# Kernel optimization log

Hardware: AMD Instinct MI355X
Metric: run time of the kernel (lower is better)

The kernel has to match this reference:

```python
import jax, jax.numpy as jnp
import numpy as np

N, E, D_IN, D, H, L, D_EMB, T = 4096, 131072, 72, 256, 8, 2, 128, 5
HD = D // H
LN_EPS = 1e-5


def _linear(x, w, b):
    # torch Linear: w is [out, in]
    return x @ w.T + b


def _layernorm(x, g, b):
    mu = jnp.mean(x, axis=-1, keepdims=True)
    var = jnp.var(x, axis=-1, keepdims=True)
    return (x - mu) * jax.lax.rsqrt(var + LN_EPS) * g + b


def _gps_layer(x, edge_index, p):
    src, dst = edge_index[0], edge_index[1]
    # GINConv: sum-aggregate neighbor messages, then MLP((1+eps)*x + agg)
    agg = jax.ops.segment_sum(x[src], dst, num_segments=N)
    h = (1.0 + p['gin_eps']) * x + agg
    h = _linear(jax.nn.elu(_linear(h, p['mlp_w1'], p['mlp_b1'])), p['mlp_w2'], p['mlp_b2'])
    h = jax.nn.elu(_layernorm(h, p['ln1_g'], p['ln1_b']))
    x = x + h

    # global multi-head self-attention over all N nodes (seq len = N)
    qkv = x @ p['attn_in_w'].T + p['attn_in_b']  # [N, 3D]
    q, k, v = jnp.split(qkv, 3, axis=-1)
    q = q.reshape(N, H, HD)
    k = k.reshape(N, H, HD)
    v = v.reshape(N, H, HD)
    scores = jnp.einsum('nhd,mhd->hnm', q, k) / np.sqrt(HD).astype(np.float32)
    attn = jax.nn.softmax(scores, axis=-1)
    o = jnp.einsum('hnm,mhd->nhd', attn, v).reshape(N, D)
    o = _linear(o, p['attn_out_w'], p['attn_out_b'])
    o = _layernorm(o, p['ln2_g'], p['ln2_b'])
    x = x + o

    # FFN (dim -> 2*dim -> dim, GELU)
    f = _linear(jax.nn.gelu(_linear(x, p['ffn_w1'], p['ffn_b1'])), p['ffn_w2'], p['ffn_b2'])
    f = _layernorm(f, p['ln3_g'], p['ln3_b'])
    return x + f


def setup_inputs() -> dict:
    key = jax.random.key(0)
    ks = iter(jax.random.split(key, 64))

    def w(shape, fan_in):
        return jax.random.normal(next(ks), shape, jnp.float32) * (1.0 / np.sqrt(fan_in))

    inp = {
        'x': jax.random.normal(next(ks), (N, D_IN), jnp.float32),
        'edge_index': jax.random.randint(next(ks), (2, E), 0, N, jnp.int64),
        'in_w': w((D, D_IN), D_IN), 'in_b': jnp.zeros((D,), jnp.float32),
        'head_w1': w((D_EMB, D), D), 'head_b1': jnp.zeros((D_EMB,), jnp.float32),
        'head_w2': w((T, D_EMB), D_EMB), 'head_b2': jnp.zeros((T,), jnp.float32),
    }
    # stacked per-layer params, leading axis L
    inp['mlp_w1'] = w((L, D, D), D); inp['mlp_b1'] = jnp.zeros((L, D), jnp.float32)
    inp['mlp_w2'] = w((L, D, D), D); inp['mlp_b2'] = jnp.zeros((L, D), jnp.float32)
    inp['gin_eps'] = jnp.zeros((L,), jnp.float32)
    inp['ln1_g'] = jnp.ones((L, D), jnp.float32); inp['ln1_b'] = jnp.zeros((L, D), jnp.float32)
    inp['attn_in_w'] = w((L, 3 * D, D), D); inp['attn_in_b'] = jnp.zeros((L, 3 * D), jnp.float32)
    inp['attn_out_w'] = w((L, D, D), D); inp['attn_out_b'] = jnp.zeros((L, D), jnp.float32)
    inp['ln2_g'] = jnp.ones((L, D), jnp.float32); inp['ln2_b'] = jnp.zeros((L, D), jnp.float32)
    inp['ffn_w1'] = w((L, 2 * D, D), D); inp['ffn_b1'] = jnp.zeros((L, 2 * D), jnp.float32)
    inp['ffn_w2'] = w((L, D, 2 * D), 2 * D); inp['ffn_b2'] = jnp.zeros((L, D), jnp.float32)
    inp['ln3_g'] = jnp.ones((L, D), jnp.float32); inp['ln3_b'] = jnp.zeros((L, D), jnp.float32)
    return inp


PER_LAYER = ['mlp_w1', 'mlp_b1', 'mlp_w2', 'mlp_b2', 'gin_eps', 'ln1_g', 'ln1_b',
             'attn_in_w', 'attn_in_b', 'attn_out_w', 'attn_out_b', 'ln2_g', 'ln2_b',
             'ffn_w1', 'ffn_b1', 'ffn_w2', 'ffn_b2', 'ln3_g', 'ln3_b']


def reference(x, edge_index, in_w, in_b, head_w1, head_b1, head_w2, head_b2,
              mlp_w1, mlp_b1, mlp_w2, mlp_b2, gin_eps, ln1_g, ln1_b,
              attn_in_w, attn_in_b, attn_out_w, attn_out_b, ln2_g, ln2_b,
              ffn_w1, ffn_b1, ffn_w2, ffn_b2, ln3_g, ln3_b):
    stacked = dict(mlp_w1=mlp_w1, mlp_b1=mlp_b1, mlp_w2=mlp_w2, mlp_b2=mlp_b2,
                   gin_eps=gin_eps, ln1_g=ln1_g, ln1_b=ln1_b,
                   attn_in_w=attn_in_w, attn_in_b=attn_in_b,
                   attn_out_w=attn_out_w, attn_out_b=attn_out_b,
                   ln2_g=ln2_g, ln2_b=ln2_b, ffn_w1=ffn_w1, ffn_b1=ffn_b1,
                   ffn_w2=ffn_w2, ffn_b2=ffn_b2, ln3_g=ln3_g, ln3_b=ln3_b)
    h = jax.nn.elu(_linear(x, in_w, in_b))  # input_proj (dropout/noise off in eval)
    for l in range(L):
        p = {k: v[l] for k, v in stacked.items()}
        h = _gps_layer(h, edge_index, p)
    out = _linear(jax.nn.elu(_linear(h, head_w1, head_b1)), head_w2, head_b2)
    return out
```

## Files before the change

### kernel.cpp

```cpp
#include <hip/hip_runtime.h>
#include <math.h>

#define NN 4096
#define NE 131072
#define DIM 256
#define NHEAD 8
#define HD 32

typedef __attribute__((ext_vector_type(8))) short short8v;
typedef __attribute__((ext_vector_type(4))) float f32x4;
#define MFMA16(a, b, c) __builtin_amdgcn_mfma_f32_16x16x32_bf16(a, b, c, 0, 0, 0)

__device__ __forceinline__ float elu_f(float v){ return v > 0.f ? v : expm1f(v); }
__device__ __forceinline__ float gelu_f(float v){
  const float c = 0.7978845608028654f;
  float t = tanhf(c * (v + 0.044715f * v * v * v));
  return 0.5f * v * (1.f + t);
}
__device__ __forceinline__ unsigned short f2bf(float f) {
  unsigned int u = __builtin_bit_cast(unsigned int, f);
  u += 0x7FFFu + ((u >> 16) & 1u);
  return (unsigned short)(u >> 16);
}
__device__ __forceinline__ float bf2f(unsigned short u) {
  return __builtin_bit_cast(float, (unsigned int)u << 16);
}
__device__ __forceinline__ unsigned int pk2(float a, float b) {
  return (unsigned int)f2bf(a) | ((unsigned int)f2bf(b) << 16);
}

__global__ void zero_counts(int* __restrict__ counts) {
  int i = blockIdx.x * 256 + threadIdx.x;
  if (i < NN) counts[i] = 0;
}

__global__ void count_edges(const int* __restrict__ ei, int* __restrict__ counts) {
  int e = blockIdx.x * 256 + threadIdx.x;
  if (e < NE) atomicAdd(&counts[ei[NE + e]], 1);
}

__global__ __launch_bounds__(1024) void scan_offsets(const int* __restrict__ counts,
                                                     int* __restrict__ offs,
                                                     int* __restrict__ cursor) {
  __shared__ int tmp[1024];
  int t = threadIdx.x;
  int base = t * 4;
  int c0 = counts[base], c1 = counts[base+1], c2 = counts[base+2], c3 = counts[base+3];
  int tsum = c0 + c1 + c2 + c3;
  tmp[t] = tsum;
  __syncthreads();
  for (int d = 1; d < 1024; d <<= 1) {
    int v = (t >= d) ? tmp[t - d] : 0;
    __syncthreads();
    tmp[t] += v;
    __syncthreads();
  }
  int excl = tmp[t] - tsum;
  offs[base]   = excl;           cursor[base]   = excl;
  offs[base+1] = excl + c0;      cursor[base+1] = excl + c0;
  offs[base+2] = excl + c0 + c1; cursor[base+2] = excl + c0 + c1;
  offs[base+3] = excl + c0 + c1 + c2; cursor[base+3] = excl + c0 + c1 + c2;
  if (t == 1023) offs[NN] = tmp[1023];
}

__global__ void scatter_edges(const int* __restrict__ ei, int* __restrict__ cursor,
                              int* __restrict__ esrc) {
  int e = blockIdx.x * 256 + threadIdx.x;
  if (e < NE) {
    int d = ei[NE + e];
    int pos = atomicAdd(&cursor[d], 1);
    esrc[pos] = ei[e];
  }
}

__global__ __launch_bounds__(256) void gin_agg(const int* __restrict__ offs,
                                               const int* __restrict__ esrc,
                                               const unsigned short* __restrict__ xb,
                                               const float* __restrict__ eps_p, int l,
                                               unsigned short* __restrict__ aggb) {
  int n = blockIdx.x, c = threadIdx.x;
  int e0 = offs[n], e1 = offs[n + 1];
  float acc = 0.f;
  for (int e = e0; e < e1; e++) acc += bf2f(xb[(size_t)esrc[e] * DIM + c]);
  float eps = eps_p[l];
  aggb[(size_t)n * DIM + c] = f2bf((1.f + eps) * bf2f(xb[(size_t)n * DIM + c]) + acc);
}

template<int ACT, int WF32, int WBF16, int QSCALE, int BK>
__global__ __launch_bounds__(256) void gemm_mfma(
    const unsigned short* __restrict__ A, const unsigned short* __restrict__ W,
    const float* __restrict__ bias, float* __restrict__ Cf,
    unsigned short* __restrict__ Cb, int M, int N, int K)
{
  __shared__ __align__(16) unsigned short As[64][BK + 8];
  __shared__ __align__(16) unsigned short Ws[32][BK + 8];
  constexpr int CPR = BK / 8;
  int t = threadIdx.x;
  int w = t >> 6, lane = t & 63, lo = lane & 15, g = lane >> 4;
  int wm = w & 1, wn = w >> 1;
  int bn = blockIdx.x * 32, bm = blockIdx.y * 64;

  f32x4 acc0 = {0.f, 0.f, 0.f, 0.f};
  f32x4 acc1 = {0.f, 0.f, 0.f, 0.f};

  for (int k0 = 0; k0 < K; k0 += BK) {
    #pragma unroll
    for (int c = 0; c < 64 * CPR; c += 256) {
      int cc = c + t;
      int row = cc / CPR, off = (cc % CPR) * 8;
      *(short8v*)&As[row][off] = *(const short8v*)(A + (size_t)(bm + row) * K + k0 + off);
    }
    {
      int cc = t;
      if (cc < 32 * CPR) {
        int row = cc / CPR, off = (cc % CPR) * 8;
        *(short8v*)&Ws[row][off] = *(const short8v*)(W + (size_t)(bn + row) * K + k0 + off);
      }
    }
    __syncthreads();
    #pragma unroll
    for (int ks = 0; ks < BK; ks += 32) {
      short8v a0 = *(const short8v*)&As[wm * 32 + lo][ks + 8 * g];
      short8v a1 = *(const short8v*)&As[wm * 32 + 16 + lo][ks + 8 * g];
      short8v b0 = *(const short8v*)&Ws[wn * 16 + lo][ks + 8 * g];
      acc0 = MFMA16(a0, b0, acc0);
      acc1 = MFMA16(a1, b0, acc1);
    }
    __syncthreads();
  }

  #pragma unroll
  for (int mi = 0; mi < 2; mi++) {
    f32x4 av = (mi == 0) ? acc0 : acc1;
    #pragma unroll
    for (int r = 0; r < 4; r++) {
      int row = bm + wm * 32 + mi * 16 + 4 * g + r;
      int col = bn + wn * 16 + lo;
      float v = av[r] + bias[col];
      if (ACT == 1) v = elu_f(v);
      if (ACT == 2) v = gelu_f(v);
      if (QSCALE) { if (col < 256) v *= 0.17677669529663687f; }
      if (WF32) Cf[(size_t)row * N + col] = v;
      if (WBF16) Cb[(size_t)row * N + col] = f2bf(v);
    }
  }
}

template<int ACT>
__global__ __launch_bounds__(256) void ln_act_add(const float* __restrict__ in,
                                                  const float* __restrict__ g,
                                                  const float* __restrict__ b,
                                                  float* __restrict__ x,
                                                  unsigned short* __restrict__ xb) {
  int rowb = blockIdx.x;
  int c = threadIdx.x;
  float v = in[(size_t)rowb * DIM + c];
  float s = v, s2 = v * v;
  #pragma unroll
  for (int off = 32; off >= 1; off >>= 1) {
    s  += __shfl_xor(s,  off, 64);
    s2 += __shfl_xor(s2, off, 64);
  }
  __shared__ float ws1[4], ws2[4];
  int w = threadIdx.x >> 6, lane = threadIdx.x & 63;
  if (lane == 0) { ws1[w] = s; ws2[w] = s2; }
  __syncthreads();
  s  = ws1[0] + ws1[1] + ws1[2] + ws1[3];
  s2 = ws2[0] + ws2[1] + ws2[2] + ws2[3];
  float mean = s * (1.f / DIM);
  float var = s2 * (1.f / DIM) - mean * mean;
  float r = rsqrtf(var + 1e-5f);
  float o = (v - mean) * r * g[c] + b[c];
  if (ACT == 1) o = elu_f(o);
  float nx = x[(size_t)rowb * DIM + c] + o;
  x[(size_t)rowb * DIM + c] = nx;
  xb[(size_t)rowb * DIM + c] = f2bf(nx);
}

__global__ __launch_bounds__(256) void vt_transpose(const unsigned short* __restrict__ tbb,
                                                    unsigned short* __restrict__ VT) {
  __shared__ unsigned short lds[128][33];
  int h = blockIdx.y;
  int nb = blockIdx.x * 128;
  int tid = threadIdx.x;
  int r8 = tid >> 5, d = tid & 31;
  #pragma unroll
  for (int i = 0; i < 16; i++) {
    int n = i * 8 + r8;
    lds[n][d] = tbb[(size_t)(nb + n) * 768 + 512 + h * 32 + d];
  }
  __syncthreads();
  int dd = tid >> 7, j = tid & 127;
  #pragma unroll
  for (int i = 0; i < 16; i++) {
    int d2 = i * 2 + dd;
    VT[((size_t)h * 32 + d2) * 4096 + nb + j] = lds[j][d2];
  }
}

__global__ __launch_bounds__(256) void attn_mfma_split(
    const unsigned short* __restrict__ qkvb, const unsigned short* __restrict__ VT,
    float* __restrict__ po, float* __restrict__ ml, int kspan) {
  __shared__ __align__(16) unsigned short Ks[2][64][40];
  __shared__ __align__(16) unsigned short Vs[2][32][72];
  int tid = threadIdx.x;
  int w = tid >> 6, lane = tid & 63;
  int lo = lane & 15, g = lane >> 4;
  int h = blockIdx.y;
  int s = blockIdx.z;
  int qb = blockIdx.x * 64 + w * 16;
  int k_lo = s * kspan, k_hi = k_lo + kspan;

  int krow = tid >> 2, kq = (tid & 3) * 8;
  int vrow = tid >> 3, vo = (tid & 7) * 8;
  const unsigned short* Kg = qkvb + 256 + h * 32;
  const unsigned short* Vg = VT + ((size_t)(h * 32 + vrow)) * 4096;

  short8v qf = *(const short8v*)(qkvb + (size_t)(qb + lo) * 768 + h * 32 + 8 * g);

  f32x4 acc0 = {0.f, 0.f, 0.f, 0.f};
  f32x4 acc1 = {0.f, 0.f, 0.f, 0.f};
  float m = -1e30f, l = 0.f;
  const f32x4 zf = {0.f, 0.f, 0.f, 0.f};

  {
    short8v rk0 = *(const short8v*)(Kg + (size_t)(k_lo + krow) * 768 + kq);
    short8v rv0 = *(const short8v*)(Vg + k_lo + vo);
    *(short8v*)&Ks[0][krow][kq] = rk0;
    *(short8v*)&Vs[0][vrow][vo] = rv0;
  }
  __syncthreads();

  int buf = 0;
  for (int kb = k_lo; kb < k_hi; kb += 64) {
    short8v rk, rv;
    bool more = (kb + 64 < k_hi);
    if (more) {
      rk = *(const short8v*)(Kg + (size_t)(kb + 64 + krow) * 768 + kq);
      rv = *(const short8v*)(Vg + kb + 64 + vo);
    }

    short8v kA0 = *(const short8v*)&Ks[buf][lo][8 * g];
    short8v kA1 = *(const short8v*)&Ks[buf][16 + lo][8 * g];
    short8v kA2 = *(const short8v*)&Ks[buf][32 + lo][8 * g];
    short8v kA3 = *(const short8v*)&Ks[buf][48 + lo][8 * g];
    f32x4 s0_ = MFMA16(kA0, qf, zf);
    f32x4 s1_ = MFMA16(kA1, qf, zf);
    f32x4 s2_ = MFMA16(kA2, qf, zf);
    f32x4 s3_ = MFMA16(kA3, qf, zf);

    float ta_ = fmaxf(fmaxf(fmaxf(s0_[0],s0_[1]), fmaxf(s0_[2],s0_[3])),
                      fmaxf(fmaxf(s1_[0],s1_[1]), fmaxf(s1_[2],s1_[3])));
    float tb_ = fmaxf(fmaxf(fmaxf(s2_[0],s2_[1]), fmaxf(s2_[2],s2_[3])),
                      fmaxf(fmaxf(s3_[0],s3_[1]), fmaxf(s3_[2],s3_[3])));
    float t_ = fmaxf(ta_, tb_);
    t_ = fmaxf(t_, __shfl_xor(t_, 16, 64));
    t_ = fmaxf(t_, __shfl_xor(t_, 32, 64));
    if (!__all(t_ <= m)) {
      float nm_ = fmaxf(m, t_);
      float f_ = __expf(m - nm_);
      m = nm_; l *= f_;
      acc0[0]*=f_; acc0[1]*=f_; acc0[2]*=f_; acc0[3]*=f_;
      acc1[0]*=f_; acc1[1]*=f_; acc1[2]*=f_; acc1[3]*=f_;
    }
    float p0_=__expf(s0_[0]-m), p1_=__expf(s0_[1]-m), p2_=__expf(s0_[2]-m), p3_=__expf(s0_[3]-m);
    float p4_=__expf(s1_[0]-m), p5_=__expf(s1_[1]-m), p6_=__expf(s1_[2]-m), p7_=__expf(s1_[3]-m);
    float p8_=__expf(s2_[0]-m), p9_=__expf(s2_[1]-m), pA_=__expf(s2_[2]-m), pB_=__expf(s2_[3]-m);
    float pC_=__expf(s3_[0]-m), pD_=__expf(s3_[1]-m), pE_=__expf(s3_[2]-m), pF_=__expf(s3_[3]-m);
    l += ((((p0_+p1_)+(p2_+p3_)) + ((p4_+p5_)+(p6_+p7_))) +
          (((p8_+p9_)+(pA_+pB_)) + ((pC_+pD_)+(pE_+pF_))));

    uint4 uA_ = { pk2(p0_,p1_), pk2(p2_,p3_), pk2(p4_,p5_), pk2(p6_,p7_) };
    uint4 uB_ = { pk2(p8_,p9_), pk2(pA_,pB_), pk2(pC_,pD_), pk2(pE_,pF_) };
    short8v pbA_ = __builtin_bit_cast(short8v, uA_);
    short8v pbB_ = __builtin_bit_cast(short8v, uB_);

    short4 Wa0 = *(const short4*)&Vs[buf][lo][4 * g];
    short4 Wa1 = *(const short4*)&Vs[buf][lo][16 + 4 * g];
    short4 Wa2 = *(const short4*)&Vs[buf][lo][32 + 4 * g];
    short4 Wa3 = *(const short4*)&Vs[buf][lo][48 + 4 * g];
    short4 Xa0 = *(const short4*)&Vs[buf][16 + lo][4 * g];
    short4 Xa1 = *(const short4*)&Vs[buf][16 + lo][16 + 4 * g];
    short4 Xa2 = *(const short4*)&Vs[buf][16 + lo][32 + 4 * g];
    short4 Xa3 = *(const short4*)&Vs[buf][16 + lo][48 + 4 * g];
    short8v va0_ = {Wa0.x,Wa0.y,Wa0.z,Wa0.w, Wa1.x,Wa1.y,Wa1.z,Wa1.w};
    short8v va1_ = {Wa2.x,Wa2.y,Wa2.z,Wa2.w, Wa3.x,Wa3.y,Wa3.z,Wa3.w};
    short8v vb0_ = {Xa0.x,Xa0.y,Xa0.z,Xa0.w, Xa1.x,Xa1.y,Xa1.z,Xa1.w};
    short8v vb1_ = {Xa2.x,Xa2.y,Xa2.z,Xa2.w, Xa3.x,Xa3.y,Xa3.z,Xa3.w};
    acc0 = MFMA16(va0_, pbA_, acc0);
    acc0 = MFMA16(va1_, pbB_, acc0);
    acc1 = MFMA16(vb0_, pbA_, acc1);
    acc1 = MFMA16(vb1_, pbB_, acc1);

    if (more) {
      *(short8v*)&Ks[buf ^ 1][krow][kq] = rk;
      *(short8v*)&Vs[buf ^ 1][vrow][vo] = rv;
    }
    __syncthreads();
    buf ^= 1;
  }

  l += __shfl_xor(l, 16, 64);
  l += __shfl_xor(l, 32, 64);

  int q = qb + lo;
  float* pr = po + ((size_t)s * NN + q) * DIM + h * 32 + 4 * g;
  *(f32x4*)pr = acc0;
  *(f32x4*)(pr + 16) = acc1;
  if (g == 0) {
    float2* mlp = (float2*)(ml + (((size_t)s * NN + q) * NHEAD + h) * 2);
    *mlp = float2{m, l};
  }
}

__global__ __launch_bounds__(256) void attn_merge(const float* __restrict__ po,
                                                  const float* __restrict__ ml,
                                                  unsigned short* __restrict__ attb, int S) {
  int q = blockIdx.x;
  int c = threadIdx.x;
  int h = c >> 5;
  float M = -1e30f;
  for (int s = 0; s < S; s++)
    M = fmaxf(M, ml[(((size_t)s * NN + q) * NHEAD + h) * 2]);
  float L = 0.f, O = 0.f;
  for (int s = 0; s < S; s++) {
    const float* mlp = ml + (((size_t)s * NN + q) * NHEAD + h) * 2;
    float e = __expf(mlp[0] - M);
    L += e * mlp[1];
    O += e * po[((size_t)s * NN + q) * DIM + c];
  }
  attb[(size_t)q * DIM + c] = f2bf(O / L);
}

#define WO0 0
#define WO1 131072
#define WO2 262144
#define WO3 655360
#define WO4 786432
#define WO5 1048576
#define WO6 1310720
#define WTOT 1343488
#define WBLK 1312
#define XPBLK 1536
#define WPBLK 96
__global__ __launch_bounds__(256) void prep_convert(
    const float* __restrict__ s0, const float* __restrict__ s1,
    const float* __restrict__ s2, const float* __restrict__ s3,
    const float* __restrict__ s4, const float* __restrict__ s5,
    const float* __restrict__ s6, unsigned short* __restrict__ dst,
    const float* __restrict__ x_in, unsigned short* __restrict__ xinb,
    const float* __restrict__ in_w, unsigned short* __restrict__ inwb) {
  int bid = blockIdx.x;
  if (bid < WBLK) {
    int i4 = (bid * 256 + threadIdx.x) * 4;
    if (i4 >= WTOT) return;
    const float* src; int loc;
    if      (i4 < WO1) { src = s0; loc = i4 - WO0; }
    else if (i4 < WO2) { src = s1; loc = i4 - WO1; }
    else if (i4 < WO3) { src = s2; loc = i4 - WO2; }
    else if (i4 < WO4) { src = s3; loc = i4 - WO3; }
    else if (i4 < WO5) { src = s4; loc = i4 - WO4; }
    else if (i4 < WO6) { src = s5; loc = i4 - WO5; }
    else               { src = s6; loc = i4 - WO6; }
    float4 v = *(const float4*)(src + loc);
    ushort4 o;
    o.x = f2bf(v.x); o.y = f2bf(v.y); o.z = f2bf(v.z); o.w = f2bf(v.w);
    *(ushort4*)(dst + i4) = o;
  } else if (bid < WBLK + XPBLK) {
    int idx = (bid - WBLK) * 256 + threadIdx.x;
    int row = idx / 96, col = idx - row * 96;
    xinb[idx] = (col < 72) ? f2bf(x_in[row * 72 + col]) : (unsigned short)0;
  } else {
    int idx = (bid - WBLK - XPBLK) * 256 + threadIdx.x;
    int row = idx / 96, col = idx - row * 96;
    inwb[idx] = (col < 72) ? f2bf(in_w[row * 72 + col]) : (unsigned short)0;
  }
}

__global__ void head2_kernel(const float* __restrict__ e, const float* __restrict__ w,
                             const float* __restrict__ b, float* __restrict__ out) {
  int idx = blockIdx.x * 256 + threadIdx.x;
  if (idx >= NN * 5) return;
  int rowi = idx / 5, col = idx % 5;
  float s = b[col];
  const float* ep = e + (size_t)rowi * 128;
  const float* wp = w + (size_t)col * 128;
  #pragma unroll 16
  for (int k = 0; k < 128; k++) s += ep[k] * wp[k];
  out[idx] = s;
}

extern "C" void kernel_launch(void* const* d_in, const int* in_sizes, int n_in,
                              void* d_out, int out_size, void* d_ws, size_t ws_size,
                              hipStream_t stream) {
  const float* x_in   = (const float*)d_in[0];
  const int*   ei     = (const int*)  d_in[1];
  const float* in_w   = (const float*)d_in[2];
  const float* in_b   = (const float*)d_in[3];
  const float* head_w1= (const float*)d_in[4];
  const float* head_b1= (const float*)d_in[5];
  const float* head_w2= (const float*)d_in[6];
  const float* head_b2= (const float*)d_in[7];
  const float* mlp_w1 = (const float*)d_in[8];
  const float* mlp_b1 = (const float*)d_in[9];
  const float* mlp_w2 = (const float*)d_in[10];
  const float* mlp_b2 = (const float*)d_in[11];
  const float* gin_eps= (const float*)d_in[12];
  const float* ln1_g  = (const float*)d_in[13];
  const float* ln1_b  = (const float*)d_in[14];
  const float* attn_in_w = (const float*)d_in[15];
  const float* attn_in_b = (const float*)d_in[16];
  const float* attn_out_w= (const float*)d_in[17];
  const float* attn_out_b= (const float*)d_in[18];
  const float* ln2_g  = (const float*)d_in[19];
  const float* ln2_b  = (const float*)d_in[20];
  const float* ffn_w1 = (const float*)d_in[21];
  const float* ffn_b1 = (const float*)d_in[22];
  const float* ffn_w2 = (const float*)d_in[23];
  const float* ffn_b2 = (const float*)d_in[24];
  const float* ln3_g  = (const float*)d_in[25];
  const float* ln3_b  = (const float*)d_in[26];

  float* ws = (float*)d_ws;
  float* x    = ws;
  float* t2   = x  + (size_t)NN * DIM;
  float* he   = t2 + (size_t)NN * DIM;
  unsigned short* xb   = (unsigned short*)(he + (size_t)NN * 128);
  unsigned short* tbb  = xb   + (size_t)NN * DIM;
  unsigned short* aggb = tbb  + (size_t)NN * 768;
  unsigned short* attb = aggb + (size_t)NN * DIM;
  unsigned short* VT   = attb + (size_t)NN * DIM;
  unsigned short* xinb = VT   + (size_t)NN * DIM;
  unsigned short* inwb = xinb + (size_t)NN * 96;
  unsigned short* warena = inwb + 256 * 96;
  int* counts = (int*)(warena + WTOT);
  int* offs   = counts + NN;
  int* cursor = offs + NN + 1;
  int* esrc   = cursor + NN;
  float* po   = (float*)(esrc + NE);
  size_t used_f = (size_t)(po - ws);
  int S = 1;
  for (int cand = 4; cand >= 2; cand >>= 1) {
    size_t need = (used_f + (size_t)cand * NN * DIM + (size_t)cand * NN * NHEAD * 2) * 4;
    if (ws_size >= need) { S = cand; break; }
  }
  float* ml = po + (size_t)S * NN * DIM;
  int kspan = NN / S;

  const unsigned short* w_mlp1 = warena + WO0;
  const unsigned short* w_mlp2 = warena + WO1;
  const unsigned short* w_qkv  = warena + WO2;
  const unsigned short* w_aout = warena + WO3;
  const unsigned short* w_ffn1 = warena + WO4;
  const unsigned short* w_ffn2 = warena + WO5;
  const unsigned short* w_h1   = warena + WO6;

  zero_counts<<<16, 256, 0, stream>>>(counts);
  count_edges<<<NE / 256, 256, 0, stream>>>(ei, counts);
  scan_offsets<<<1, 1024, 0, stream>>>(counts, offs, cursor);
  scatter_edges<<<NE / 256, 256, 0, stream>>>(ei, cursor, esrc);

  prep_convert<<<WBLK + XPBLK + WPBLK, 256, 0, stream>>>(
      mlp_w1, mlp_w2, attn_in_w, attn_out_w, ffn_w1, ffn_w2, head_w1, warena,
      x_in, xinb, in_w, inwb);

  gemm_mfma<1,1,1,0,32><<<dim3(DIM/32, NN/64), 256, 0, stream>>>(xinb, inwb, in_b, x, xb,
                                                                 NN, DIM, 96);

  for (int l = 0; l < 2; l++) {
    gin_agg<<<NN, 256, 0, stream>>>(offs, esrc, xb, gin_eps, l, aggb);
    gemm_mfma<1,0,1,0,64><<<dim3(8, 64), 256, 0, stream>>>(aggb, w_mlp1 + (size_t)l*65536,
                                                           mlp_b1 + l*DIM, nullptr, tbb,
                                                           NN, DIM, DIM);
    gemm_mfma<0,1,0,0,64><<<dim3(8, 64), 256, 0, stream>>>(tbb, w_mlp2 + (size_t)l*65536,
                                                           mlp_b2 + l*DIM, t2, nullptr,
                                                           NN, DIM, DIM);
    ln_act_add<1><<<NN, 256, 0, stream>>>(t2, ln1_g + l*DIM, ln1_b + l*DIM, x, xb);

    gemm_mfma<0,0,1,1,64><<<dim3(24, 64), 256, 0, stream>>>(xb, w_qkv + (size_t)l*196608,
                                                            attn_in_b + l*768, nullptr, tbb,
                                                            NN, 768, DIM);
    vt_transpose<<<dim3(32, 8), 256, 0, stream>>>(tbb, VT);
    attn_mfma_split<<<dim3(64, NHEAD, S), 256, 0, stream>>>(tbb, VT, po, ml, kspan);
    attn_merge<<<NN, 256, 0, stream>>>(po, ml, attb, S);
    gemm_mfma<0,1,0,0,64><<<dim3(8, 64), 256, 0, stream>>>(attb, w_aout + (size_t)l*65536,
                                                           attn_out_b + l*DIM, t2, nullptr,
                                                           NN, DIM, DIM);
    ln_act_add<0><<<NN, 256, 0, stream>>>(t2, ln2_g + l*DIM, ln2_b + l*DIM, x, xb);

    gemm_mfma<2,0,1,0,64><<<dim3(16, 64), 256, 0, stream>>>(xb, w_ffn1 + (size_t)l*131072,
                                                            ffn_b1 + l*512, nullptr, tbb,
                                                            NN, 512, DIM);
    gemm_mfma<0,1,0,0,64><<<dim3(8, 64), 256, 0, stream>>>(tbb, w_ffn2 + (size_t)l*131072,
                                                           ffn_b2 + l*DIM, t2, nullptr,
                                                           NN, DIM, 512);
    ln_act_add<0><<<NN, 256, 0, stream>>>(t2, ln3_g + l*DIM, ln3_b + l*DIM, x, xb);
  }

  gemm_mfma<1,1,0,0,64><<<dim3(4, 64), 256, 0, stream>>>(xb, w_h1, head_b1, he, nullptr,
                                                         NN, 128, DIM);
  head2_kernel<<<(NN * 5 + 255) / 256, 256, 0, stream>>>(he, head_w2, head_b2, (float*)d_out);
}
```

Baseline: 353.2 us.

## Double-buffer GEMM tiles, use packed bf16 convert, allow 8-way attention split

The GEMM kernel now prefetches the next K tile into registers and stores it into a second shared-memory buffer while the current tile is being multiplied, so each tile needs one barrier instead of two. The attention probability packing switches to the HIP packed float2-to-bf16 intrinsic, which may map to a hardware convert instruction instead of manual rounding. The split-K factor for attention may now go up to 8 when the workspace allows it, giving more parallelism at the cost of a bigger merge step. Double buffering doubles GEMM shared memory and adds register pressure.

```diff
diff --git a/kernel.cpp b/kernel.cpp
--- a/kernel.cpp
+++ b/kernel.cpp
@@ -1,4 +1,5 @@
 #include <hip/hip_runtime.h>
+#include <hip/hip_bf16.h>
 #include <math.h>
 
 #define NN 4096
@@ -25,8 +26,11 @@
 __device__ __forceinline__ float bf2f(unsigned short u) {
   return __builtin_bit_cast(float, (unsigned int)u << 16);
 }
-__device__ __forceinline__ unsigned int pk2(float a, float b) {
-  return (unsigned int)f2bf(a) | ((unsigned int)f2bf(b) << 16);
+__device__ __forceinline__ unsigned int pk2c(float a, float b) {
+  __hip_bfloat162 h = __float22bfloat162_rn(float2{a, b});
+  unsigned int r;
+  __builtin_memcpy(&r, &h, 4);
+  return r;
 }
 
 __global__ void zero_counts(int* __restrict__ counts) {
@@ -92,9 +96,13 @@
     const float* __restrict__ bias, float* __restrict__ Cf,
     unsigned short* __restrict__ Cb, int M, int N, int K)
 {
-  __shared__ __align__(16) unsigned short As[64][BK + 8];
-  __shared__ __align__(16) unsigned short Ws[32][BK + 8];
+  __shared__ __align__(16) unsigned short As[2][64][BK + 8];
+  __shared__ __align__(16) unsigned short Ws[2][32][BK + 8];
   constexpr int CPR = BK / 8;
+  constexpr int ACH = 64 * CPR;
+  constexpr int WCH = 32 * CPR;
+  constexpr int NA = (ACH + 255) / 256;
+  constexpr int NW = (WCH + 255) / 256;
   int t = threadIdx.x;
   int w = t >> 6, lane = t & 63, lo = lane & 15, g = lane >> 4;
   int wm = w & 1, wn = w >> 1;
@@ -102,31 +110,60 @@
 
   f32x4 acc0 = {0.f, 0.f, 0.f, 0.f};
   f32x4 acc1 = {0.f, 0.f, 0.f, 0.f};
-
+  short8v pa[NA], pw[NW];
+
+  auto LOADG = [&](int k0) {
+    #pragma unroll
+    for (int i = 0; i < NA; i++) {
+      int cc = i * 256 + t;
+      int row = cc / CPR, off = (cc % CPR) * 8;
+      pa[i] = *(const short8v*)(A + (size_t)(bm + row) * K + k0 + off);
+    }
+    #pragma unroll
+    for (int i = 0; i < NW; i++) {
+      int cc = i * 256 + t;
+      if (cc < WCH) {
+        int row = cc / CPR, off = (cc % CPR) * 8;
+        pw[i] = *(const short8v*)(W + (size_t)(bn + row) * K + k0 + off);
+      }
+    }
+  };
+  auto STORE = [&](int b) {
+    #pragma unroll
+    for (int i = 0; i < NA; i++) {
+      int cc = i * 256 + t;
+      int row = cc / CPR, off = (cc % CPR) * 8;
+      *(short8v*)&As[b][row][off] = pa[i];
+    }
+    #pragma unroll
+    for (int i = 0; i < NW; i++) {
+      int cc = i * 256 + t;
+      if (cc < WCH) {
+        int row = cc / CPR, off = (cc % CPR) * 8;
+        *(short8v*)&Ws[b][row][off] = pw[i];
+      }
+    }
+  };
+
+  LOADG(0);
+  STORE(0);
+  __syncthreads();
+
+  int buf = 0;
   for (int k0 = 0; k0 < K; k0 += BK) {
-    #pragma unroll
-    for (int c = 0; c < 64 * CPR; c += 256) {
-      int cc = c + t;
-      int row = cc / CPR, off = (cc % CPR) * 8;
-      *(short8v*)&As[row][off] = *(const short8v*)(A + (size_t)(bm + row) * K + k0 + off);
-    }
-    {
-      int cc = t;
-      if (cc < 32 * CPR) {
-        int row = cc / CPR, off = (cc % CPR) * 8;
-        *(short8v*)&Ws[row][off] = *(const short8v*)(W + (size_t)(bn + row) * K + k0 + off);
-      }
-    }
-    __syncthreads();
+    bool more = (k0 + BK < K);
+    if (more) LOADG(k0 + BK);
     #pragma unroll
     for (int ks = 0; ks < BK; ks += 32) {
-      short8v a0 = *(const short8v*)&As[wm * 32 + lo][ks + 8 * g];
-      short8v a1 = *(const short8v*)&As[wm * 32 + 16 + lo][ks + 8 * g];
-      short8v b0 = *(const short8v*)&Ws[wn * 16 + lo][ks + 8 * g];
+      short8v a0 = *(const short8v*)&As[buf][wm * 32 + lo][ks + 8 * g];
+      short8v a1 = *(const short8v*)&As[buf][wm * 32 + 16 + lo][ks + 8 * g];
+      short8v b0 = *(const short8v*)&Ws[buf][wn * 16 + lo][ks + 8 * g];
       acc0 = MFMA16(a0, b0, acc0);
       acc1 = MFMA16(a1, b0, acc1);
     }
+    if (more) STORE(buf ^ 1);
     __syncthreads();
+    buf ^= 1;
   }
 
   #pragma unroll
@@ -270,8 +307,8 @@
     l += ((((p0_+p1_)+(p2_+p3_)) + ((p4_+p5_)+(p6_+p7_))) +
           (((p8_+p9_)+(pA_+pB_)) + ((pC_+pD_)+(pE_+pF_))));
 
-    uint4 uA_ = { pk2(p0_,p1_), pk2(p2_,p3_), pk2(p4_,p5_), pk2(p6_,p7_) };
-    uint4 uB_ = { pk2(p8_,p9_), pk2(pA_,pB_), pk2(pC_,pD_), pk2(pE_,pF_) };
+    uint4 uA_ = { pk2c(p0_,p1_), pk2c(p2_,p3_), pk2c(p4_,p5_), pk2c(p6_,p7_) };
+    uint4 uB_ = { pk2c(p8_,p9_), pk2c(pA_,pB_), pk2c(pC_,pD_), pk2c(pE_,pF_) };
     short8v pbA_ = __builtin_bit_cast(short8v, uA_);
     short8v pbB_ = __builtin_bit_cast(short8v, uB_);
 
@@ -440,7 +477,7 @@
   float* po   = (float*)(esrc + NE);
   size_t used_f = (size_t)(po - ws);
   int S = 1;
-  for (int cand = 4; cand >= 2; cand >>= 1) {
+  for (int cand = 8; cand >= 2; cand >>= 1) {
     size_t need = (used_f + (size_t)cand * NN * DIM + (size_t)cand * NN * NHEAD * 2) * 4;
     if (ws_size >= need) { S = cand; break; }
   }
```

New measurement: 347.2 us. Within noise of the previous version (-1.7%).
